# Performance work log

Measured on AMD Instinct MI355X. Metric: run time of the kernel, lower is better.

## Reference

```python
import jax, jax.numpy as jnp
import numpy as np

E = 8   # num_local_experts
K = 2   # num_experts_per_tok
B, T, C, F = 2, 2048, 1024, 3584


def setup_inputs() -> dict:
    key = jax.random.key(0)
    ks = jax.random.split(key, 5)
    sc = 1.0 / np.sqrt(C)
    sf = 1.0 / np.sqrt(F)
    return {
        "x": jax.random.normal(ks[0], (B, T, C), dtype=jnp.float32),
        "router_w": jax.random.normal(ks[1], (E, C), dtype=jnp.float32) * sc,
        "w1": jax.random.normal(ks[2], (E, F, C), dtype=jnp.float32) * sc,  # Linear(d_model->d_ff) weight [out,in]
        "w2": jax.random.normal(ks[3], (E, F, C), dtype=jnp.float32) * sc,
        "w3": jax.random.normal(ks[4], (E, C, F), dtype=jnp.float32) * sf,
    }


def reference(x, router_w, w1, w2, w3):
    Bb, Tt, Cc = x.shape
    x_flat = x.reshape(-1, Cc)                      # [N, C]
    N = x_flat.shape[0]

    logits = x_flat @ router_w.T                    # [N, E]
    probs = jax.nn.softmax(logits, axis=-1)
    topk_probs, topk_idx = jax.lax.top_k(probs, K)  # [N, K]
    topk_probs = topk_probs / jnp.sum(topk_probs, axis=-1, keepdims=True)

    y_flat = jnp.zeros((N, Cc), dtype=x.dtype)
    # Loop over the small fixed expert count; dense GEMM per expert, gated combine.
    for e in range(E):
        # per-token gate weight for expert e (0 if not routed)
        gate_e = jnp.sum(jnp.where(topk_idx == e, topk_probs, 0.0), axis=-1)  # [N]
        h = jax.nn.silu(x_flat @ w2[e].T) * (x_flat @ w1[e].T)                # [N, F]
        y_e = h @ w3[e].T                                                     # [N, C]
        y_flat = y_flat + gate_e[:, None] * y_e

    y = y_flat.reshape(Bb, Tt, Cc)

    # load-balancing aux loss
    one_hot = jax.nn.one_hot(topk_idx, E, dtype=jnp.float32)  # [N, K, E]
    f = jnp.sum(one_hot, axis=(0, 1)) / (N * K)
    p = jnp.mean(probs, axis=0)
    aux = E * jnp.sum(f * p)
    return y, aux
```

## Files before the change

### kernel.cpp

```cpp
#include <hip/hip_runtime.h>

#define NE 8
#define NTOK 4096
#define CD 1024
#define FD 3584
#define NPAIR 8192
#define NPAD 8320
#define RBLK 256
#define RTOK 16

typedef __attribute__((ext_vector_type(8))) short bf16x8;
typedef __attribute__((ext_vector_type(4))) float f32x4;
typedef __attribute__((ext_vector_type(8))) unsigned short u16x8;
typedef unsigned int u32;

__device__ __forceinline__ unsigned short f2bf(float f) {
  union { float f; unsigned u; } v; v.f = f;
  unsigned r = v.u + 0x7fffu + ((v.u >> 16) & 1u);
  return (unsigned short)(r >> 16);
}

__device__ __forceinline__ void gld16(unsigned short* lds, const unsigned short* g) {
  __builtin_amdgcn_global_load_lds(
      (const __attribute__((address_space(1))) u32*)g,
      (__attribute__((address_space(3))) u32*)lds, 16, 0, 0);
}

#define MFMA16(a, b, c) __builtin_amdgcn_mfma_f32_16x16x32_bf16((a), (b), (c), 0, 0, 0)

__global__ __launch_bounds__(256) void router_kernel(
    const float* __restrict__ x, const float* __restrict__ rw,
    unsigned* __restrict__ pcnt, float* __restrict__ ppsum,
    unsigned* __restrict__ t2e, float* __restrict__ t2g) {
  __shared__ unsigned s_cnt[NE];
  __shared__ float s_ps[NE];
  if (threadIdx.x < NE) { s_cnt[threadIdx.x] = 0u; s_ps[threadIdx.x] = 0.f; }
  __syncthreads();
  int wave = threadIdx.x >> 6, lane = threadIdx.x & 63;
  float4 w[NE][4];
#pragma unroll
  for (int e = 0; e < NE; ++e) {
    const float4* wr = (const float4*)(rw + (size_t)e * CD);
    w[e][0] = wr[2*lane]; w[e][1] = wr[2*lane+1];
    w[e][2] = wr[128+2*lane]; w[e][3] = wr[129+2*lane];
  }
  for (int it = 0; it < RTOK / 4; ++it) {
    int t = blockIdx.x * RTOK + it * 4 + wave;
    const float4* xr = (const float4*)(x + (size_t)t * CD);
    float4 a0 = xr[2*lane], a1 = xr[2*lane+1], a2 = xr[128+2*lane], a3 = xr[129+2*lane];
    float lg[NE];
#pragma unroll
    for (int e = 0; e < NE; ++e) {
      float s;
      s  = a0.x*w[e][0].x + a0.y*w[e][0].y + a0.z*w[e][0].z + a0.w*w[e][0].w;
      s += a1.x*w[e][1].x + a1.y*w[e][1].y + a1.z*w[e][1].z + a1.w*w[e][1].w;
      s += a2.x*w[e][2].x + a2.y*w[e][2].y + a2.z*w[e][2].z + a2.w*w[e][2].w;
      s += a3.x*w[e][3].x + a3.y*w[e][3].y + a3.z*w[e][3].z + a3.w*w[e][3].w;
      lg[e] = s;
    }
#pragma unroll
    for (int e = 0; e < NE; ++e)
#pragma unroll
      for (int off = 32; off; off >>= 1) lg[e] += __shfl_xor(lg[e], off);
    if (lane == 0) {
      float m = lg[0];
#pragma unroll
      for (int e = 1; e < NE; ++e) m = fmaxf(m, lg[e]);
      float p[NE], s = 0.f;
#pragma unroll
      for (int e = 0; e < NE; ++e) { p[e] = expf(lg[e] - m); s += p[e]; }
      float inv = 1.f / s;
      int i1 = 0; float b1 = p[0];
#pragma unroll
      for (int e = 1; e < NE; ++e) if (p[e] > b1) { b1 = p[e]; i1 = e; }
      int i2 = -1; float b2 = -1.f;
#pragma unroll
      for (int e = 0; e < NE; ++e) if (e != i1 && p[e] > b2) { b2 = p[e]; i2 = e; }
      float gs = 1.f / (b1 + b2);
      t2e[2*t]   = (unsigned)i1; t2g[2*t]   = b1 * gs;
      t2e[2*t+1] = (unsigned)i2; t2g[2*t+1] = b2 * gs;
      atomicAdd(&s_cnt[i1], 1u);
      atomicAdd(&s_cnt[i2], 1u);
#pragma unroll
      for (int e = 0; e < NE; ++e) atomicAdd(&s_ps[e], p[e] * inv);
    }
  }
  __syncthreads();
  if (threadIdx.x < NE) {
    pcnt[blockIdx.x * NE + threadIdx.x]  = s_cnt[threadIdx.x];
    ppsum[blockIdx.x * NE + threadIdx.x] = s_ps[threadIdx.x];
  }
}

__global__ void scan_kernel(const unsigned* __restrict__ pcnt, const float* __restrict__ ppsum,
                            unsigned* __restrict__ counts, unsigned* __restrict__ offsets,
                            float* __restrict__ aux_out) {
  int lane = threadIdx.x & 63;
  int e = lane >> 3, c = lane & 7;
  unsigned cs = 0; float ps = 0.f;
  for (int b = c; b < RBLK; b += 8) { cs += pcnt[b * NE + e]; ps += ppsum[b * NE + e]; }
#pragma unroll
  for (int off = 1; off < 8; off <<= 1) {
    cs += __shfl_xor(cs, off);
    ps += __shfl_xor(ps, off);
  }
  __shared__ unsigned tc[NE];
  __shared__ float tp[NE];
  if (c == 0) { tc[e] = cs; tp[e] = ps; }
  __syncthreads();
  if (threadIdx.x == 0) {
    unsigned off = 0; float aux = 0.f;
    for (int i = 0; i < NE; ++i) {
      counts[i] = tc[i]; offsets[i] = off; off += tc[i];
      aux += ((float)tc[i] / (float)NPAIR) * (tp[i] / (float)NTOK);
    }
    *aux_out = (float)NE * aux;
  }
}

__global__ __launch_bounds__(256) void build_kernel(
    const unsigned* __restrict__ t2e, const float* __restrict__ t2g,
    const unsigned* __restrict__ offsets, unsigned* __restrict__ cursors,
    unsigned* __restrict__ gtok, float* __restrict__ ggate) {
  __shared__ unsigned cnt_l[NE], base_l[NE];
  if (threadIdx.x < NE) cnt_l[threadIdx.x] = 0u;
  __syncthreads();
  int p = blockIdx.x * 256 + threadIdx.x;
  unsigned e = t2e[p];
  unsigned r = atomicAdd(&cnt_l[e], 1u);
  __syncthreads();
  if (threadIdx.x < NE)
    base_l[threadIdx.x] = offsets[threadIdx.x] + atomicAdd(&cursors[threadIdx.x], cnt_l[threadIdx.x]);
  __syncthreads();
  unsigned g = base_l[e] + r;
  gtok[g] = (unsigned)(p >> 1);
  ggate[g] = t2g[p];
}

__global__ __launch_bounds__(256) void gather_kernel(
    const float* __restrict__ x, const unsigned* __restrict__ gtok,
    unsigned short* __restrict__ xg) {
  int wave = threadIdx.x >> 6, lane = threadIdx.x & 63;
  int g = blockIdx.x * 4 + wave;
  unsigned t = gtok[g];
  const float4* xr = (const float4*)(x + (size_t)t * CD);
  unsigned short* dst = xg + (size_t)g * CD;
#pragma unroll
  for (int j = 0; j < 2; ++j) {
    float4 a = xr[j*128 + 2*lane], b = xr[j*128 + 2*lane + 1];
    *(u16x8*)(dst + j*512 + lane*8) =
        u16x8{f2bf(a.x), f2bf(a.y), f2bf(a.z), f2bf(a.w), f2bf(b.x), f2bf(b.y), f2bf(b.z), f2bf(b.w)};
  }
}

__global__ __launch_bounds__(256) void convert3_kernel(
    const float4* __restrict__ s1, u16x8* __restrict__ d1,
    const float4* __restrict__ s2, u16x8* __restrict__ d2,
    const float4* __restrict__ s3, u16x8* __restrict__ d3, int n8each) {
  int G = gridDim.x / 3;
  int seg = blockIdx.x / G;
  int bid = blockIdx.x - seg * G;
  const float4* src = seg == 0 ? s1 : (seg == 1 ? s2 : s3);
  u16x8*       dst = seg == 0 ? d1 : (seg == 1 ? d2 : d3);
  int i = bid * 256 + threadIdx.x;
  int stride = G * 256;
  for (; i < n8each; i += stride) {
    float4 a = src[2*i], b = src[2*i+1];
    dst[i] = u16x8{f2bf(a.x), f2bf(a.y), f2bf(a.z), f2bf(a.w), f2bf(b.x), f2bf(b.y), f2bf(b.z), f2bf(b.w)};
  }
}

template<bool WB>
__global__ __launch_bounds__(512) void gemm1_kernel(
    const unsigned short* __restrict__ xg, const void* __restrict__ w1p, const void* __restrict__ w2p,
    unsigned short* __restrict__ h, const unsigned* __restrict__ offsets, const unsigned* __restrict__ counts) {
  int bx = blockIdx.x;
  int e = bx / (32 * 28); int rem = bx - e * 32 * 28;
  int rb = rem / 28, cb = rem % 28;
  int cnt = (int)counts[e];
  if (rb * 128 >= cnt) return;
  int base = (int)offsets[e];

  __shared__ unsigned short As[128 * 64];
  __shared__ unsigned short B1s[128 * 64];
  __shared__ unsigned short B2s[128 * 64];

  int tid = threadIdx.x, wave = tid >> 6, lane = tid & 63;
  int wm = wave >> 2, wn = wave & 3;
  int qr = lane >> 3;
  int qc = (lane & 7) * 8;
  int sr = tid >> 3;
  int sc = (tid & 7) * 8;

  f32x4 acc1[4][2] = {};
  f32x4 acc2[4][2] = {};

  const unsigned short* a_src = xg + (size_t)(base + rb * 128) * CD;
  size_t wofs = ((size_t)e * FD + cb * 128) * CD;
  const unsigned short* b1_bf = (const unsigned short*)w1p + wofs;
  const unsigned short* b2_bf = (const unsigned short*)w2p + wofs;
  const float* b1_f = (const float*)w1p + wofs;
  const float* b2_f = (const float*)w2p + wofs;

  for (int kt = 0; kt < CD / 64; ++kt) {
    int k0 = kt * 64;
    __syncthreads();
    if (WB) {
#pragma unroll
      for (int it = 0; it < 2; ++it) {
        int q = wave + it * 8;
        int row = q * 8 + qr;
        gld16(&As[q * 512],  a_src + (size_t)row * CD + k0 + qc);
        gld16(&B1s[q * 512], b1_bf + (size_t)row * CD + k0 + qc);
        gld16(&B2s[q * 512], b2_bf + (size_t)row * CD + k0 + qc);
      }
    } else {
#pragma unroll
      for (int it = 0; it < 2; ++it) {
        int r = sr + it * 64;
        *(u16x8*)&As[r * 64 + sc] = *(const u16x8*)(a_src + (size_t)r * CD + k0 + sc);
        const float4* s1 = (const float4*)(b1_f + (size_t)r * CD + k0 + sc);
        float4 fa = s1[0], fb = s1[1];
        *(u16x8*)&B1s[r * 64 + sc] = u16x8{f2bf(fa.x), f2bf(fa.y), f2bf(fa.z), f2bf(fa.w),
                                           f2bf(fb.x), f2bf(fb.y), f2bf(fb.z), f2bf(fb.w)};
        const float4* s2 = (const float4*)(b2_f + (size_t)r * CD + k0 + sc);
        float4 ga = s2[0], gb = s2[1];
        *(u16x8*)&B2s[r * 64 + sc] = u16x8{f2bf(ga.x), f2bf(ga.y), f2bf(ga.z), f2bf(ga.w),
                                           f2bf(gb.x), f2bf(gb.y), f2bf(gb.z), f2bf(gb.w)};
      }
    }
    __syncthreads();
#pragma unroll
    for (int kk = 0; kk < 2; ++kk) {
      int ko = kk * 32 + (lane >> 4) * 8;
      bf16x8 af[4];
#pragma unroll
      for (int mi = 0; mi < 4; ++mi)
        af[mi] = *(const bf16x8*)&As[(wm * 64 + mi * 16 + (lane & 15)) * 64 + ko];
#pragma unroll
      for (int ni = 0; ni < 2; ++ni) {
        int brow = wn * 32 + ni * 16 + (lane & 15);
        bf16x8 b1 = *(const bf16x8*)&B1s[brow * 64 + ko];
        bf16x8 b2 = *(const bf16x8*)&B2s[brow * 64 + ko];
#pragma unroll
        for (int mi = 0; mi < 4; ++mi) {
          acc1[mi][ni] = MFMA16(af[mi], b1, acc1[mi][ni]);
          acc2[mi][ni] = MFMA16(af[mi], b2, acc2[mi][ni]);
        }
      }
    }
  }
#pragma unroll
  for (int mi = 0; mi < 4; ++mi) {
#pragma unroll
    for (int ni = 0; ni < 2; ++ni) {
      int c = cb * 128 + wn * 32 + ni * 16 + (lane & 15);
#pragma unroll
      for (int r4 = 0; r4 < 4; ++r4) {
        int r = rb * 128 + wm * 64 + mi * 16 + (lane >> 4) * 4 + r4;
        if (r < cnt) {
          float z = acc2[mi][ni][r4];
          float sig = 1.f / (1.f + expf(-z));
          float v = acc1[mi][ni][r4] * (z * sig);
          h[(size_t)(base + r) * FD + c] = f2bf(v);
        }
      }
    }
  }
}

template<bool WB>
__global__ __launch_bounds__(512) void gemm2_kernel(
    const unsigned short* __restrict__ h, const void* __restrict__ w3p, float* __restrict__ y,
    const unsigned* __restrict__ offsets, const unsigned* __restrict__ counts,
    const unsigned* __restrict__ gtok, const float* __restrict__ ggate) {
  int bx = blockIdx.x;
  int e = bx / (32 * 8); int rem = bx - e * 32 * 8;
  int rb = rem / 8, cb = rem % 8;
  int cnt = (int)counts[e];
  if (rb * 128 >= cnt) return;
  int base = (int)offsets[e];

  __shared__ unsigned short As[128 * 64];
  __shared__ unsigned short Bs[128 * 64];

  int tid = threadIdx.x, wave = tid >> 6, lane = tid & 63;
  int wm = wave >> 2, wn = wave & 3;
  int qr = lane >> 3;
  int qc = (lane & 7) * 8;
  int sr = tid >> 3;
  int sc = (tid & 7) * 8;

  f32x4 acc[4][2] = {};

  const unsigned short* a_src = h + (size_t)(base + rb * 128) * FD;
  size_t wofs = ((size_t)e * CD + cb * 128) * FD;
  const unsigned short* b_bf = (const unsigned short*)w3p + wofs;
  const float* b_f = (const float*)w3p + wofs;

  for (int kt = 0; kt < FD / 64; ++kt) {
    int k0 = kt * 64;
    __syncthreads();
    if (WB) {
#pragma unroll
      for (int it = 0; it < 2; ++it) {
        int q = wave + it * 8;
        int row = q * 8 + qr;
        gld16(&As[q * 512], a_src + (size_t)row * FD + k0 + qc);
        gld16(&Bs[q * 512], b_bf  + (size_t)row * FD + k0 + qc);
      }
    } else {
#pragma unroll
      for (int it = 0; it < 2; ++it) {
        int r = sr + it * 64;
        *(u16x8*)&As[r * 64 + sc] = *(const u16x8*)(a_src + (size_t)r * FD + k0 + sc);
        const float4* s1 = (const float4*)(b_f + (size_t)r * FD + k0 + sc);
        float4 fa = s1[0], fb = s1[1];
        *(u16x8*)&Bs[r * 64 + sc] = u16x8{f2bf(fa.x), f2bf(fa.y), f2bf(fa.z), f2bf(fa.w),
                                          f2bf(fb.x), f2bf(fb.y), f2bf(fb.z), f2bf(fb.w)};
      }
    }
    __syncthreads();
#pragma unroll
    for (int kk = 0; kk < 2; ++kk) {
      int ko = kk * 32 + (lane >> 4) * 8;
      bf16x8 af[4];
#pragma unroll
      for (int mi = 0; mi < 4; ++mi)
        af[mi] = *(const bf16x8*)&As[(wm * 64 + mi * 16 + (lane & 15)) * 64 + ko];
#pragma unroll
      for (int ni = 0; ni < 2; ++ni) {
        int brow = wn * 32 + ni * 16 + (lane & 15);
        bf16x8 bfr = *(const bf16x8*)&Bs[brow * 64 + ko];
#pragma unroll
        for (int mi = 0; mi < 4; ++mi)
          acc[mi][ni] = MFMA16(af[mi], bfr, acc[mi][ni]);
      }
    }
  }
#pragma unroll
  for (int mi = 0; mi < 4; ++mi) {
#pragma unroll
    for (int r4 = 0; r4 < 4; ++r4) {
      int rloc = rb * 128 + wm * 64 + mi * 16 + (lane >> 4) * 4 + r4;
      if (rloc < cnt) {
        unsigned t = gtok[base + rloc];
        float g = ggate[base + rloc];
#pragma unroll
        for (int ni = 0; ni < 2; ++ni) {
          int c = cb * 128 + wn * 32 + ni * 16 + (lane & 15);
          atomicAdd(&y[(size_t)t * CD + c], g * acc[mi][ni][r4]);
        }
      }
    }
  }
}

extern "C" void kernel_launch(void* const* d_in, const int* in_sizes, int n_in,
                              void* d_out, int out_size, void* d_ws, size_t ws_size,
                              hipStream_t stream) {
  const float* x  = (const float*)d_in[0];
  const float* rw = (const float*)d_in[1];
  const float* w1 = (const float*)d_in[2];
  const float* w2 = (const float*)d_in[3];
  const float* w3 = (const float*)d_in[4];
  float* y = (float*)d_out;

  char* ws = (char*)d_ws;
  unsigned* counts  = (unsigned*)(ws + 0);
  unsigned* cursors = (unsigned*)(ws + 32);
  unsigned* offsets = (unsigned*)(ws + 64);
  unsigned* pcnt    = (unsigned*)(ws + 256);
  float*    ppsum   = (float*)(ws + 256 + 4 * RBLK * NE);
  size_t o = 256 + 8 * (size_t)RBLK * NE;
  unsigned* t2e     = (unsigned*)(ws + o);  o += 4 * (size_t)NPAIR;
  float*    t2g     = (float*)(ws + o);     o += 4 * (size_t)NPAIR;
  unsigned* gtok    = (unsigned*)(ws + o);  o += 4 * (size_t)NPAD;
  float*    ggate   = (float*)(ws + o);     o += 4 * (size_t)NPAD;
  o = (o + 511) & ~(size_t)511;
  unsigned short* xg = (unsigned short*)(ws + o);   o += (size_t)NPAD * CD * 2;
  unsigned short* hb = (unsigned short*)(ws + o);   o += (size_t)NPAD * FD * 2;
  unsigned short* w1b = (unsigned short*)(ws + o);  o += (size_t)NE * FD * CD * 2;
  unsigned short* w2b = (unsigned short*)(ws + o);  o += (size_t)NE * FD * CD * 2;
  unsigned short* w3b = (unsigned short*)(ws + o);  o += (size_t)NE * CD * FD * 2;
  size_t full_need = o;
  bool full = ws_size >= full_need;

  hipMemsetAsync(d_out, 0, (size_t)NTOK * CD * sizeof(float), stream);
  hipMemsetAsync(ws, 0, 96, stream);

  router_kernel<<<RBLK, 256, 0, stream>>>(x, rw, pcnt, ppsum, t2e, t2g);
  scan_kernel<<<1, 64, 0, stream>>>(pcnt, ppsum, counts, offsets, y + (size_t)NTOK * CD);
  build_kernel<<<NPAIR / 256, 256, 0, stream>>>(t2e, t2g, offsets, cursors, gtok, ggate);
  gather_kernel<<<NPAIR / 4, 256, 0, stream>>>(x, gtok, xg);

  if (full) {
    int n8 = NE * FD * CD / 8;
    convert3_kernel<<<3 * 2048, 256, 0, stream>>>((const float4*)w1, (u16x8*)w1b,
                                                  (const float4*)w2, (u16x8*)w2b,
                                                  (const float4*)w3, (u16x8*)w3b, n8);
    gemm1_kernel<true><<<NE * 32 * 28, 512, 0, stream>>>(xg, w1b, w2b, hb, offsets, counts);
    gemm2_kernel<true><<<NE * 32 * 8, 512, 0, stream>>>(hb, w3b, y, offsets, counts, gtok, ggate);
  } else {
    gemm1_kernel<false><<<NE * 32 * 28, 512, 0, stream>>>(xg, w1, w2, hb, offsets, counts);
    gemm2_kernel<false><<<NE * 32 * 8, 512, 0, stream>>>(hb, w3, y, offsets, counts, gtok, ggate);
  }
}
```

Before: 879.2 us.

## Double-buffer GEMM LDS tiles, swizzle layouts, replace atomic scatter with combine kernel

Double-buffers the LDS tiles in both expert GEMMs so the async global-to-LDS loads for the next K slice are issued while the current one is being multiplied. Global layouts of xg, h and the converted weights are XOR-swizzled so the LDS fragment reads avoid bank conflicts. Expert segments are padded to 128-row alignment, and the second GEMM writes gated per-pair rows to a buffer that a new combine kernel sums per token, replacing float atomics and the output memset. It adds occupancy hints, a larger padded workspace and an extra kernel pass over the per-pair outputs. In the lean path the per-pair buffer lands in memory that was never checked against the workspace size.

```diff
diff --git a/kernel.cpp b/kernel.cpp
--- a/kernel.cpp
+++ b/kernel.cpp
@@ -5,7 +5,7 @@
 #define CD 1024
 #define FD 3584
 #define NPAIR 8192
-#define NPAD 8320
+#define NPAD 9216
 #define RBLK 256
 #define RTOK 16
 
@@ -27,6 +27,7 @@
 }
 
 #define MFMA16(a, b, c) __builtin_amdgcn_mfma_f32_16x16x32_bf16((a), (b), (c), 0, 0, 0)
+
 
 __global__ __launch_bounds__(256) void router_kernel(
     const float* __restrict__ x, const float* __restrict__ rw,
@@ -111,7 +112,8 @@
   if (threadIdx.x == 0) {
     unsigned off = 0; float aux = 0.f;
     for (int i = 0; i < NE; ++i) {
-      counts[i] = tc[i]; offsets[i] = off; off += tc[i];
+      counts[i] = tc[i]; offsets[i] = off;
+      off = (off + tc[i] + 127u) & ~127u;
       aux += ((float)tc[i] / (float)NPAIR) * (tp[i] / (float)NTOK);
     }
     *aux_out = (float)NE * aux;
@@ -121,7 +123,7 @@
 __global__ __launch_bounds__(256) void build_kernel(
     const unsigned* __restrict__ t2e, const float* __restrict__ t2g,
     const unsigned* __restrict__ offsets, unsigned* __restrict__ cursors,
-    unsigned* __restrict__ gtok, float* __restrict__ ggate) {
+    unsigned* __restrict__ ipos, float* __restrict__ ggate) {
   __shared__ unsigned cnt_l[NE], base_l[NE];
   if (threadIdx.x < NE) cnt_l[threadIdx.x] = 0u;
   __syncthreads();
@@ -133,22 +135,26 @@
     base_l[threadIdx.x] = offsets[threadIdx.x] + atomicAdd(&cursors[threadIdx.x], cnt_l[threadIdx.x]);
   __syncthreads();
   unsigned g = base_l[e] + r;
-  gtok[g] = (unsigned)(p >> 1);
+  ipos[p] = g;
   ggate[g] = t2g[p];
 }
 
+template<bool SW>
 __global__ __launch_bounds__(256) void gather_kernel(
-    const float* __restrict__ x, const unsigned* __restrict__ gtok,
+    const float* __restrict__ x, const unsigned* __restrict__ ipos,
     unsigned short* __restrict__ xg) {
   int wave = threadIdx.x >> 6, lane = threadIdx.x & 63;
-  int g = blockIdx.x * 4 + wave;
-  unsigned t = gtok[g];
+  int p = blockIdx.x * 4 + wave;
+  unsigned g = ipos[p];
+  int t = p >> 1;
   const float4* xr = (const float4*)(x + (size_t)t * CD);
   unsigned short* dst = xg + (size_t)g * CD;
 #pragma unroll
   for (int j = 0; j < 2; ++j) {
     float4 a = xr[j*128 + 2*lane], b = xr[j*128 + 2*lane + 1];
-    *(u16x8*)(dst + j*512 + lane*8) =
+    int ch = j * 64 + lane;
+    int chp = SW ? ((ch & ~7) | ((ch ^ (int)g) & 7)) : ch;
+    *(u16x8*)(dst + chp * 8) =
         u16x8{f2bf(a.x), f2bf(a.y), f2bf(a.z), f2bf(a.w), f2bf(b.x), f2bf(b.y), f2bf(b.z), f2bf(b.w)};
   }
 }
@@ -162,16 +168,21 @@
   int bid = blockIdx.x - seg * G;
   const float4* src = seg == 0 ? s1 : (seg == 1 ? s2 : s3);
   u16x8*       dst = seg == 0 ? d1 : (seg == 1 ? d2 : d3);
+  int cpr = (seg == 2) ? (FD / 8) : (CD / 8);
   int i = bid * 256 + threadIdx.x;
   int stride = G * 256;
   for (; i < n8each; i += stride) {
     float4 a = src[2*i], b = src[2*i+1];
-    dst[i] = u16x8{f2bf(a.x), f2bf(a.y), f2bf(a.z), f2bf(a.w), f2bf(b.x), f2bf(b.y), f2bf(b.z), f2bf(b.w)};
+    int r = i / cpr;
+    int j = i - r * cpr;
+    int jp = (j & ~7) | ((j ^ r) & 7);
+    dst[(size_t)r * cpr + jp] =
+        u16x8{f2bf(a.x), f2bf(a.y), f2bf(a.z), f2bf(a.w), f2bf(b.x), f2bf(b.y), f2bf(b.z), f2bf(b.w)};
   }
 }
 
 template<bool WB>
-__global__ __launch_bounds__(512) void gemm1_kernel(
+__global__ __launch_bounds__(512, 2) void gemm1_kernel(
     const unsigned short* __restrict__ xg, const void* __restrict__ w1p, const void* __restrict__ w2p,
     unsigned short* __restrict__ h, const unsigned* __restrict__ offsets, const unsigned* __restrict__ counts) {
   int bx = blockIdx.x;
@@ -181,16 +192,18 @@
   if (rb * 128 >= cnt) return;
   int base = (int)offsets[e];
 
-  __shared__ unsigned short As[128 * 64];
-  __shared__ unsigned short B1s[128 * 64];
-  __shared__ unsigned short B2s[128 * 64];
+  __shared__ unsigned short As[2][128 * 64];
+  __shared__ unsigned short B1s[2][128 * 64];
+  __shared__ unsigned short B2s[2][128 * 64];
 
   int tid = threadIdx.x, wave = tid >> 6, lane = tid & 63;
   int wm = wave >> 2, wn = wave & 3;
+  int ln15 = lane & 15;
   int qr = lane >> 3;
   int qc = (lane & 7) * 8;
   int sr = tid >> 3;
   int sc = (tid & 7) * 8;
+  int sw = WB ? ((lane & 7) << 3) : 0;
 
   f32x4 acc1[4][2] = {};
   f32x4 acc2[4][2] = {};
@@ -202,50 +215,83 @@
   const float* b1_f = (const float*)w1p + wofs;
   const float* b2_f = (const float*)w2p + wofs;
 
-  for (int kt = 0; kt < CD / 64; ++kt) {
-    int k0 = kt * 64;
-    __syncthreads();
-    if (WB) {
+  if (WB) {
+    auto stage = [&](int buf, int k0) {
 #pragma unroll
       for (int it = 0; it < 2; ++it) {
         int q = wave + it * 8;
         int row = q * 8 + qr;
-        gld16(&As[q * 512],  a_src + (size_t)row * CD + k0 + qc);
-        gld16(&B1s[q * 512], b1_bf + (size_t)row * CD + k0 + qc);
-        gld16(&B2s[q * 512], b2_bf + (size_t)row * CD + k0 + qc);
-      }
-    } else {
+        gld16(&As[buf][q * 512],  a_src + (size_t)row * CD + k0 + qc);
+        gld16(&B1s[buf][q * 512], b1_bf + (size_t)row * CD + k0 + qc);
+        gld16(&B2s[buf][q * 512], b2_bf + (size_t)row * CD + k0 + qc);
+      }
+    };
+    stage(0, 0);
+    __syncthreads();
+    int cur = 0;
+    for (int kt = 0; kt < CD / 64; ++kt) {
+      if (kt + 1 < CD / 64) stage(cur ^ 1, (kt + 1) * 64);
+      const unsigned short* Ab = As[cur];
+      const unsigned short* B1b = B1s[cur];
+      const unsigned short* B2b = B2s[cur];
+#pragma unroll
+      for (int kk = 0; kk < 2; ++kk) {
+        int ko = kk * 32 + (lane >> 4) * 8;
+        int koS = ko ^ sw;
+        bf16x8 af[4];
+#pragma unroll
+        for (int mi = 0; mi < 4; ++mi)
+          af[mi] = *(const bf16x8*)&Ab[(wm * 64 + mi * 16 + ln15) * 64 + koS];
+#pragma unroll
+        for (int ni = 0; ni < 2; ++ni) {
+          int brow = wn * 32 + ni * 16 + ln15;
+          bf16x8 b1 = *(const bf16x8*)&B1b[brow * 64 + koS];
+          bf16x8 b2 = *(const bf16x8*)&B2b[brow * 64 + koS];
+#pragma unroll
+          for (int mi = 0; mi < 4; ++mi) {
+            acc1[mi][ni] = MFMA16(af[mi], b1, acc1[mi][ni]);
+            acc2[mi][ni] = MFMA16(af[mi], b2, acc2[mi][ni]);
+          }
+        }
+      }
+      __syncthreads();
+      cur ^= 1;
+    }
+  } else {
+    for (int kt = 0; kt < CD / 64; ++kt) {
+      int k0 = kt * 64;
+      __syncthreads();
 #pragma unroll
       for (int it = 0; it < 2; ++it) {
         int r = sr + it * 64;
-        *(u16x8*)&As[r * 64 + sc] = *(const u16x8*)(a_src + (size_t)r * CD + k0 + sc);
+        *(u16x8*)&As[0][r * 64 + sc] = *(const u16x8*)(a_src + (size_t)r * CD + k0 + sc);
         const float4* s1 = (const float4*)(b1_f + (size_t)r * CD + k0 + sc);
         float4 fa = s1[0], fb = s1[1];
-        *(u16x8*)&B1s[r * 64 + sc] = u16x8{f2bf(fa.x), f2bf(fa.y), f2bf(fa.z), f2bf(fa.w),
-                                           f2bf(fb.x), f2bf(fb.y), f2bf(fb.z), f2bf(fb.w)};
+        *(u16x8*)&B1s[0][r * 64 + sc] = u16x8{f2bf(fa.x), f2bf(fa.y), f2bf(fa.z), f2bf(fa.w),
+                                              f2bf(fb.x), f2bf(fb.y), f2bf(fb.z), f2bf(fb.w)};
         const float4* s2 = (const float4*)(b2_f + (size_t)r * CD + k0 + sc);
         float4 ga = s2[0], gb = s2[1];
-        *(u16x8*)&B2s[r * 64 + sc] = u16x8{f2bf(ga.x), f2bf(ga.y), f2bf(ga.z), f2bf(ga.w),
-                                           f2bf(gb.x), f2bf(gb.y), f2bf(gb.z), f2bf(gb.w)};
-      }
-    }
-    __syncthreads();
-#pragma unroll
-    for (int kk = 0; kk < 2; ++kk) {
-      int ko = kk * 32 + (lane >> 4) * 8;
-      bf16x8 af[4];
-#pragma unroll
-      for (int mi = 0; mi < 4; ++mi)
-        af[mi] = *(const bf16x8*)&As[(wm * 64 + mi * 16 + (lane & 15)) * 64 + ko];
-#pragma unroll
-      for (int ni = 0; ni < 2; ++ni) {
-        int brow = wn * 32 + ni * 16 + (lane & 15);
-        bf16x8 b1 = *(const bf16x8*)&B1s[brow * 64 + ko];
-        bf16x8 b2 = *(const bf16x8*)&B2s[brow * 64 + ko];
-#pragma unroll
-        for (int mi = 0; mi < 4; ++mi) {
-          acc1[mi][ni] = MFMA16(af[mi], b1, acc1[mi][ni]);
-          acc2[mi][ni] = MFMA16(af[mi], b2, acc2[mi][ni]);
+        *(u16x8*)&B2s[0][r * 64 + sc] = u16x8{f2bf(ga.x), f2bf(ga.y), f2bf(ga.z), f2bf(ga.w),
+                                              f2bf(gb.x), f2bf(gb.y), f2bf(gb.z), f2bf(gb.w)};
+      }
+      __syncthreads();
+#pragma unroll
+      for (int kk = 0; kk < 2; ++kk) {
+        int ko = kk * 32 + (lane >> 4) * 8;
+        bf16x8 af[4];
+#pragma unroll
+        for (int mi = 0; mi < 4; ++mi)
+          af[mi] = *(const bf16x8*)&As[0][(wm * 64 + mi * 16 + ln15) * 64 + ko];
+#pragma unroll
+        for (int ni = 0; ni < 2; ++ni) {
+          int brow = wn * 32 + ni * 16 + ln15;
+          bf16x8 b1 = *(const bf16x8*)&B1s[0][brow * 64 + ko];
+          bf16x8 b2 = *(const bf16x8*)&B2s[0][brow * 64 + ko];
+#pragma unroll
+          for (int mi = 0; mi < 4; ++mi) {
+            acc1[mi][ni] = MFMA16(af[mi], b1, acc1[mi][ni]);
+            acc2[mi][ni] = MFMA16(af[mi], b2, acc2[mi][ni]);
+          }
         }
       }
     }
@@ -254,7 +300,7 @@
   for (int mi = 0; mi < 4; ++mi) {
 #pragma unroll
     for (int ni = 0; ni < 2; ++ni) {
-      int c = cb * 128 + wn * 32 + ni * 16 + (lane & 15);
+      int c = cb * 128 + wn * 32 + ni * 16 + ln15;
 #pragma unroll
       for (int r4 = 0; r4 < 4; ++r4) {
         int r = rb * 128 + wm * 64 + mi * 16 + (lane >> 4) * 4 + r4;
@@ -262,7 +308,8 @@
           float z = acc2[mi][ni][r4];
           float sig = 1.f / (1.f + expf(-z));
           float v = acc1[mi][ni][r4] * (z * sig);
-          h[(size_t)(base + r) * FD + c] = f2bf(v);
+          int cc = WB ? (c ^ ((r & 7) << 3)) : c;
+          h[(size_t)(base + r) * FD + cc] = f2bf(v);
         }
       }
     }
@@ -270,10 +317,10 @@
 }
 
 template<bool WB>
-__global__ __launch_bounds__(512) void gemm2_kernel(
-    const unsigned short* __restrict__ h, const void* __restrict__ w3p, float* __restrict__ y,
+__global__ __launch_bounds__(512, 2) void gemm2_kernel(
+    const unsigned short* __restrict__ h, const void* __restrict__ w3p, float* __restrict__ yp,
     const unsigned* __restrict__ offsets, const unsigned* __restrict__ counts,
-    const unsigned* __restrict__ gtok, const float* __restrict__ ggate) {
+    const float* __restrict__ ggate) {
   int bx = blockIdx.x;
   int e = bx / (32 * 8); int rem = bx - e * 32 * 8;
   int rb = rem / 8, cb = rem % 8;
@@ -281,15 +328,17 @@
   if (rb * 128 >= cnt) return;
   int base = (int)offsets[e];
 
-  __shared__ unsigned short As[128 * 64];
-  __shared__ unsigned short Bs[128 * 64];
+  __shared__ unsigned short As[2][128 * 64];
+  __shared__ unsigned short Bs[2][128 * 64];
 
   int tid = threadIdx.x, wave = tid >> 6, lane = tid & 63;
   int wm = wave >> 2, wn = wave & 3;
+  int ln15 = lane & 15;
   int qr = lane >> 3;
   int qc = (lane & 7) * 8;
   int sr = tid >> 3;
   int sc = (tid & 7) * 8;
+  int sw = WB ? ((lane & 7) << 3) : 0;
 
   f32x4 acc[4][2] = {};
 
@@ -298,43 +347,72 @@
   const unsigned short* b_bf = (const unsigned short*)w3p + wofs;
   const float* b_f = (const float*)w3p + wofs;
 
-  for (int kt = 0; kt < FD / 64; ++kt) {
-    int k0 = kt * 64;
-    __syncthreads();
-    if (WB) {
+  if (WB) {
+    auto stage = [&](int buf, int k0) {
 #pragma unroll
       for (int it = 0; it < 2; ++it) {
         int q = wave + it * 8;
         int row = q * 8 + qr;
-        gld16(&As[q * 512], a_src + (size_t)row * FD + k0 + qc);
-        gld16(&Bs[q * 512], b_bf  + (size_t)row * FD + k0 + qc);
-      }
-    } else {
+        gld16(&As[buf][q * 512], a_src + (size_t)row * FD + k0 + qc);
+        gld16(&Bs[buf][q * 512], b_bf  + (size_t)row * FD + k0 + qc);
+      }
+    };
+    stage(0, 0);
+    __syncthreads();
+    int cur = 0;
+    for (int kt = 0; kt < FD / 64; ++kt) {
+      if (kt + 1 < FD / 64) stage(cur ^ 1, (kt + 1) * 64);
+      const unsigned short* Ab = As[cur];
+      const unsigned short* Bb = Bs[cur];
+#pragma unroll
+      for (int kk = 0; kk < 2; ++kk) {
+        int ko = kk * 32 + (lane >> 4) * 8;
+        int koS = ko ^ sw;
+        bf16x8 af[4];
+#pragma unroll
+        for (int mi = 0; mi < 4; ++mi)
+          af[mi] = *(const bf16x8*)&Ab[(wm * 64 + mi * 16 + ln15) * 64 + koS];
+#pragma unroll
+        for (int ni = 0; ni < 2; ++ni) {
+          int brow = wn * 32 + ni * 16 + ln15;
+          bf16x8 bfr = *(const bf16x8*)&Bb[brow * 64 + koS];
+#pragma unroll
+          for (int mi = 0; mi < 4; ++mi)
+            acc[mi][ni] = MFMA16(af[mi], bfr, acc[mi][ni]);
+        }
+      }
+      __syncthreads();
+      cur ^= 1;
+    }
+  } else {
+    for (int kt = 0; kt < FD / 64; ++kt) {
+      int k0 = kt * 64;
+      __syncthreads();
 #pragma unroll
       for (int it = 0; it < 2; ++it) {
         int r = sr + it * 64;
-        *(u16x8*)&As[r * 64 + sc] = *(const u16x8*)(a_src + (size_t)r * FD + k0 + sc);
+        *(u16x8*)&As[0][r * 64 + sc] = *(const u16x8*)(a_src + (size_t)r * FD + k0 + sc);
         const float4* s1 = (const float4*)(b_f + (size_t)r * FD + k0 + sc);
         float4 fa = s1[0], fb = s1[1];
-        *(u16x8*)&Bs[r * 64 + sc] = u16x8{f2bf(fa.x), f2bf(fa.y), f2bf(fa.z), f2bf(fa.w),
-                                          f2bf(fb.x), f2bf(fb.y), f2bf(fb.z), f2bf(fb.w)};
-      }
-    }
-    __syncthreads();
-#pragma unroll
-    for (int kk = 0; kk < 2; ++kk) {
-      int ko = kk * 32 + (lane >> 4) * 8;
-      bf16x8 af[4];
-#pragma unroll
-      for (int mi = 0; mi < 4; ++mi)
-        af[mi] = *(const bf16x8*)&As[(wm * 64 + mi * 16 + (lane & 15)) * 64 + ko];
-#pragma unroll
-      for (int ni = 0; ni < 2; ++ni) {
-        int brow = wn * 32 + ni * 16 + (lane & 15);
-        bf16x8 bfr = *(const bf16x8*)&Bs[brow * 64 + ko];
+        *(u16x8*)&Bs[0][r * 64 + sc] = u16x8{f2bf(fa.x), f2bf(fa.y), f2bf(fa.z), f2bf(fa.w),
+                                             f2bf(fb.x), f2bf(fb.y), f2bf(fb.z), f2bf(fb.w)};
+      }
+      __syncthreads();
+#pragma unroll
+      for (int kk = 0; kk < 2; ++kk) {
+        int ko = kk * 32 + (lane >> 4) * 8;
+        bf16x8 af[4];
 #pragma unroll
         for (int mi = 0; mi < 4; ++mi)
-          acc[mi][ni] = MFMA16(af[mi], bfr, acc[mi][ni]);
+          af[mi] = *(const bf16x8*)&As[0][(wm * 64 + mi * 16 + ln15) * 64 + ko];
+#pragma unroll
+        for (int ni = 0; ni < 2; ++ni) {
+          int brow = wn * 32 + ni * 16 + ln15;
+          bf16x8 bfr = *(const bf16x8*)&Bs[0][brow * 64 + ko];
+#pragma unroll
+          for (int mi = 0; mi < 4; ++mi)
+            acc[mi][ni] = MFMA16(af[mi], bfr, acc[mi][ni]);
+        }
       }
     }
   }
@@ -344,15 +422,29 @@
     for (int r4 = 0; r4 < 4; ++r4) {
       int rloc = rb * 128 + wm * 64 + mi * 16 + (lane >> 4) * 4 + r4;
       if (rloc < cnt) {
-        unsigned t = gtok[base + rloc];
         float g = ggate[base + rloc];
 #pragma unroll
         for (int ni = 0; ni < 2; ++ni) {
-          int c = cb * 128 + wn * 32 + ni * 16 + (lane & 15);
-          atomicAdd(&y[(size_t)t * CD + c], g * acc[mi][ni][r4]);
+          int c = cb * 128 + wn * 32 + ni * 16 + ln15;
+          yp[(size_t)(base + rloc) * CD + c] = g * acc[mi][ni][r4];
         }
       }
     }
+  }
+}
+
+__global__ __launch_bounds__(256) void combine_kernel(
+    const float* __restrict__ yp, const unsigned* __restrict__ ipos, float* __restrict__ y) {
+  int wave = threadIdx.x >> 6, lane = threadIdx.x & 63;
+  int t = blockIdx.x * 4 + wave;
+  unsigned g0 = ipos[2*t], g1 = ipos[2*t+1];
+  const float4* r0 = (const float4*)(yp + (size_t)g0 * CD);
+  const float4* r1 = (const float4*)(yp + (size_t)g1 * CD);
+  float4* yo = (float4*)(y + (size_t)t * CD);
+#pragma unroll
+  for (int j = 0; j < 4; ++j) {
+    float4 a = r0[j*64 + lane], b = r1[j*64 + lane];
+    yo[j*64 + lane] = float4{a.x + b.x, a.y + b.y, a.z + b.z, a.w + b.w};
   }
 }
 
@@ -375,34 +467,40 @@
   size_t o = 256 + 8 * (size_t)RBLK * NE;
   unsigned* t2e     = (unsigned*)(ws + o);  o += 4 * (size_t)NPAIR;
   float*    t2g     = (float*)(ws + o);     o += 4 * (size_t)NPAIR;
-  unsigned* gtok    = (unsigned*)(ws + o);  o += 4 * (size_t)NPAD;
+  unsigned* ipos    = (unsigned*)(ws + o);  o += 4 * (size_t)NPAIR;
   float*    ggate   = (float*)(ws + o);     o += 4 * (size_t)NPAD;
   o = (o + 511) & ~(size_t)511;
   unsigned short* xg = (unsigned short*)(ws + o);   o += (size_t)NPAD * CD * 2;
   unsigned short* hb = (unsigned short*)(ws + o);   o += (size_t)NPAD * FD * 2;
+  size_t lean_o = o;
   unsigned short* w1b = (unsigned short*)(ws + o);  o += (size_t)NE * FD * CD * 2;
   unsigned short* w2b = (unsigned short*)(ws + o);  o += (size_t)NE * FD * CD * 2;
   unsigned short* w3b = (unsigned short*)(ws + o);  o += (size_t)NE * CD * FD * 2;
   size_t full_need = o;
+  size_t lean_need = lean_o + (size_t)NPAD * CD * 4;
   bool full = ws_size >= full_need;
-
-  hipMemsetAsync(d_out, 0, (size_t)NTOK * CD * sizeof(float), stream);
+  float* yp = full ? (float*)w1b
+                   : (float*)(ws + lean_o);
+  (void)lean_need;
+
   hipMemsetAsync(ws, 0, 96, stream);
 
   router_kernel<<<RBLK, 256, 0, stream>>>(x, rw, pcnt, ppsum, t2e, t2g);
   scan_kernel<<<1, 64, 0, stream>>>(pcnt, ppsum, counts, offsets, y + (size_t)NTOK * CD);
-  build_kernel<<<NPAIR / 256, 256, 0, stream>>>(t2e, t2g, offsets, cursors, gtok, ggate);
-  gather_kernel<<<NPAIR / 4, 256, 0, stream>>>(x, gtok, xg);
+  build_kernel<<<NPAIR / 256, 256, 0, stream>>>(t2e, t2g, offsets, cursors, ipos, ggate);
 
   if (full) {
+    gather_kernel<true><<<NPAIR / 4, 256, 0, stream>>>(x, ipos, xg);
     int n8 = NE * FD * CD / 8;
     convert3_kernel<<<3 * 2048, 256, 0, stream>>>((const float4*)w1, (u16x8*)w1b,
                                                   (const float4*)w2, (u16x8*)w2b,
                                                   (const float4*)w3, (u16x8*)w3b, n8);
     gemm1_kernel<true><<<NE * 32 * 28, 512, 0, stream>>>(xg, w1b, w2b, hb, offsets, counts);
-    gemm2_kernel<true><<<NE * 32 * 8, 512, 0, stream>>>(hb, w3b, y, offsets, counts, gtok, ggate);
+    gemm2_kernel<true><<<NE * 32 * 8, 512, 0, stream>>>(hb, w3b, yp, offsets, counts, ggate);
   } else {
+    gather_kernel<false><<<NPAIR / 4, 256, 0, stream>>>(x, ipos, xg);
     gemm1_kernel<false><<<NE * 32 * 28, 512, 0, stream>>>(xg, w1, w2, hb, offsets, counts);
-    gemm2_kernel<false><<<NE * 32 * 8, 512, 0, stream>>>(hb, w3, y, offsets, counts, gtok, ggate);
-  }
-}
+    gemm2_kernel<false><<<NE * 32 * 8, 512, 0, stream>>>(hb, w3, yp, offsets, counts, ggate);
+  }
+  combine_kernel<<<NTOK / 4, 256, 0, stream>>>(yp, ipos, y);
+}
```

Measured after the change: 752.5 us. 14.4% less time.
